# Performance work log

Measured on AMD Instinct MI355X. Metric: run time of the kernel, lower is better.

The kernel has to match this reference:

```python
import jax, jax.numpy as jnp
import numpy as np

HEAD_NUM = 4
EMB = 128
N_NODES = 50000
N_EDGES = 600000


def setup_inputs() -> dict:
    key = jax.random.key(0)
    k1, k2, k3, k4, k5, k6 = jax.random.split(key, 6)
    embeds = jax.random.normal(k1, (N_NODES, EMB), dtype=jnp.float32)
    qW = jax.random.normal(k2, (EMB, EMB), dtype=jnp.float32) * (1.0 / np.sqrt(EMB))
    kW = jax.random.normal(k3, (EMB, EMB), dtype=jnp.float32) * (1.0 / np.sqrt(EMB))
    vW = jax.random.normal(k4, (EMB, EMB), dtype=jnp.float32) * (1.0 / np.sqrt(EMB))
    rows = jax.random.randint(k5, (N_EDGES,), 0, N_NODES, dtype=jnp.int32)
    cols = jax.random.randint(k6, (N_EDGES,), 0, N_NODES, dtype=jnp.int32)
    return {"embeds": embeds, "qW": qW, "kW": kW, "vW": vW,
            "rows": rows, "cols": cols, "n_nodes": N_NODES}


def reference(embeds, qW, kW, vW, rows, cols, n_nodes):
    H = HEAD_NUM
    D = embeds.shape[1]
    Dh = D // H
    rowEmb = embeds[rows]                                   # [E, D] gather
    colEmb = embeds[cols]                                   # [E, D] gather
    q = (rowEmb @ qW).reshape(-1, H, Dh)                    # [E, H, Dh]
    k = (colEmb @ kW).reshape(-1, H, Dh)
    v = (colEmb @ vW).reshape(-1, H, Dh)
    att = jnp.einsum('ehd,ehd->eh', q, k)                   # per-edge per-head logits
    att = jnp.clip(att, -10.0, 10.0)
    expAtt = jnp.exp(att)                                   # [E, H]
    attNorm = jax.ops.segment_sum(expAtt, rows, num_segments=n_nodes)  # [N, H]
    att = expAtt / (attNorm[rows] + 1e-8)                   # segment softmax
    res = (att[..., None] * v).reshape(-1, D)               # [E, D]
    out = jax.ops.segment_sum(res, rows, num_segments=n_nodes)  # [N, D]
    return out
```

## Files before the change

kernel.cpp:

```cpp
#include <hip/hip_runtime.h>
#include <math.h>

#define EMB 128
#define HEADS 4
#define ROWSTRIDE 152
#define OSTRIDE2 388
#define CAP 64
#define CLAMP_L2 14.4269504088896f

typedef __attribute__((ext_vector_type(8))) _Float16 f16x8;
typedef __attribute__((ext_vector_type(4))) _Float16 f16x4;
typedef __attribute__((ext_vector_type(2))) _Float16 f16x2;
typedef __attribute__((ext_vector_type(4))) float f32x4;

__global__ __launch_bounds__(256) void prep_w(
    const float* __restrict__ Wq, const float* __restrict__ Wk, const float* __restrict__ Wv,
    _Float16* __restrict__ Wfrag)
{
    int flat = blockIdx.x * 256 + threadIdx.x;
    int m    = flat >> 14;
    int rem  = flat & 16383;
    int ct   = rem >> 11;
    int s    = (rem >> 9) & 3;
    int lane = (rem >> 3) & 63;
    int j    = rem & 7;
    int k = s * 32 + (lane >> 4) * 8 + j;
    int n = ct * 16 + (lane & 15);
    const float* Ws[3] = { Wq, Wk, Wv };
    float val = Ws[m][k * 128 + n];
    if (m == 0) val *= 1.44269504088896f;
    Wfrag[flat] = (_Float16)val;
}

__global__ __launch_bounds__(256) void mega_kernel(
    const float* __restrict__ embeds,
    const _Float16* __restrict__ Wfrag,
    _Float16* __restrict__ Qh, _Float16* __restrict__ KV,
    const int* __restrict__ rows, const int* __restrict__ cols,
    int* __restrict__ deg, unsigned short* __restrict__ slots,
    int N, int E, int PB, int S)
{
    __shared__ __align__(16) _Float16 sBuf[64 * OSTRIDE2];

    const int bid = blockIdx.x;
    const bool isProj = ((bid % S) == 0) && ((bid / S) < PB);

    if (!isProj) {
        int fidx = bid - min((bid + S - 1) / S, PB);
        int e = fidx * 256 + threadIdx.x;
        if (e < E) {
            int r = rows[e];
            int pos = atomicAdd(&deg[r], 1);
            if (pos < CAP) slots[(size_t)r * CAP + pos] = (unsigned short)cols[e];
        }
        return;
    }

    const int n0 = (bid / S) * 64;
    const int t  = threadIdx.x;

    #pragma unroll
    for (int j = 0; j < 8; j++) {
        int flat = t + j * 256;
        int row  = flat >> 5;
        int c4   = flat & 31;
        int gn   = n0 + row;
        float4 v = (gn < N) ? reinterpret_cast<const float4*>(embeds)[(size_t)gn * 32 + c4]
                            : make_float4(0.f, 0.f, 0.f, 0.f);
        f16x4 u = { (_Float16)v.x, (_Float16)v.y, (_Float16)v.z, (_Float16)v.w };
        *reinterpret_cast<f16x4*>(&sBuf[row * ROWSTRIDE + c4 * 4]) = u;
    }
    __syncthreads();

    const int w    = t >> 6;
    const int lane = t & 63;
    const int nlo  = lane & 15;
    const int quad = lane >> 4;

    f16x8 a[4][4];
    #pragma unroll
    for (int strip = 0; strip < 4; strip++)
        #pragma unroll
        for (int s = 0; s < 4; s++)
            a[strip][s] = *reinterpret_cast<const f16x8*>(
                &sBuf[(16 * strip + nlo) * ROWSTRIDE + s * 32 + quad * 8]);
    __syncthreads();

    const int rbase = quad * 4;

    #pragma unroll
    for (int u = 0; u < 6; u++) {
        const int T  = w + u * 4;
        const int m  = T >> 3;
        const int ct = T & 7;

        f16x8 b[4];
        #pragma unroll
        for (int s = 0; s < 4; s++)
            b[s] = *reinterpret_cast<const f16x8*>(
                Wfrag + ((size_t)(T * 4 + s) * 64 + lane) * 8);

        const int col  = ct * 16 + nlo;
        const int lcol = (m == 0) ? col
                                  : 128 + 8 * (col >> 2) + (col & 3) + ((m == 2) ? 4 : 0);

        #pragma unroll
        for (int strip = 0; strip < 4; strip++) {
            f32x4 acc = { 0.f, 0.f, 0.f, 0.f };
            #pragma unroll
            for (int s = 0; s < 4; s++)
                acc = __builtin_amdgcn_mfma_f32_16x16x32_f16(a[strip][s], b[s], acc, 0, 0, 0);
            const int row = 16 * strip + rbase;
            #pragma unroll
            for (int r = 0; r < 4; r++)
                sBuf[(row + r) * OSTRIDE2 + lcol] = (_Float16)acc[r];
        }
    }
    __syncthreads();

    #pragma unroll
    for (int j = 0; j < 4; j++) {
        int flat = j * 2048 + t * 8;
        int row  = flat >> 7;
        int col  = flat & 127;
        int gn   = n0 + row;
        if (gn < N) {
            f16x8 v = *reinterpret_cast<const f16x8*>(&sBuf[row * OSTRIDE2 + col]);
            *reinterpret_cast<f16x8*>(&Qh[(size_t)gn * EMB + col]) = v;
        }
    }
    #pragma unroll
    for (int j = 0; j < 8; j++) {
        int flat = j * 2048 + t * 8;
        int row  = flat >> 8;
        int col  = flat & 255;
        int gn   = n0 + row;
        if (gn < N) {
            f16x8 v = *reinterpret_cast<const f16x8*>(&sBuf[row * OSTRIDE2 + 128 + col]);
            *reinterpret_cast<f16x8*>(&KV[(size_t)gn * 256 + col]) = v;
        }
    }
}

__global__ __launch_bounds__(256) void node_fused(
    const _Float16* __restrict__ Qh, const _Float16* __restrict__ KV,
    const int* __restrict__ deg, const unsigned short* __restrict__ slots,
    float* __restrict__ out, int N)
{
    int n = blockIdx.x * 8 + (threadIdx.x >> 5);
    if (n >= N) return;
    int lane = threadIdx.x & 31;

    f16x4 qh = *reinterpret_cast<const f16x4*>(Qh + (size_t)n * EMB + lane * 4);
    f16x2 q01 = { qh.x, qh.y };
    f16x2 q23 = { qh.z, qh.w };

    int cnt = deg[n];
    if (cnt > CAP) cnt = CAP;
    const unsigned short* sl = slots + (size_t)n * CAP;
    const char* KVb = (const char*)KV;
    const unsigned loff = (unsigned)lane * 16u;

    float4 acc = make_float4(0.f, 0.f, 0.f, 0.f);
    float norm = 0.f;
    int i = 0;

    for (; i + 4 <= cnt; i += 4) {
        uint2 s4 = *reinterpret_cast<const uint2*>(sl + i);
        unsigned o0 = ((s4.x & 0xffffu) << 9) + loff;
        unsigned o1 = ((s4.x >> 16)     << 9) + loff;
        unsigned o2 = ((s4.y & 0xffffu) << 9) + loff;
        unsigned o3 = ((s4.y >> 16)     << 9) + loff;
        f16x8 kv0 = *reinterpret_cast<const f16x8*>(KVb + o0);
        f16x8 kv1 = *reinterpret_cast<const f16x8*>(KVb + o1);
        f16x8 kv2 = *reinterpret_cast<const f16x8*>(KVb + o2);
        f16x8 kv3 = *reinterpret_cast<const f16x8*>(KVb + o3);

        f16x2 k0a = __builtin_shufflevector(kv0, kv0, 0, 1);
        f16x2 k0b = __builtin_shufflevector(kv0, kv0, 2, 3);
        f16x2 k1a = __builtin_shufflevector(kv1, kv1, 0, 1);
        f16x2 k1b = __builtin_shufflevector(kv1, kv1, 2, 3);
        f16x2 k2a = __builtin_shufflevector(kv2, kv2, 0, 1);
        f16x2 k2b = __builtin_shufflevector(kv2, kv2, 2, 3);
        f16x2 k3a = __builtin_shufflevector(kv3, kv3, 0, 1);
        f16x2 k3b = __builtin_shufflevector(kv3, kv3, 2, 3);

        float d0 = __builtin_amdgcn_fdot2(k0a, q01, __builtin_amdgcn_fdot2(k0b, q23, 0.f, false), false);
        float d1 = __builtin_amdgcn_fdot2(k1a, q01, __builtin_amdgcn_fdot2(k1b, q23, 0.f, false), false);
        float d2 = __builtin_amdgcn_fdot2(k2a, q01, __builtin_amdgcn_fdot2(k2b, q23, 0.f, false), false);
        float d3 = __builtin_amdgcn_fdot2(k3a, q01, __builtin_amdgcn_fdot2(k3b, q23, 0.f, false), false);

        d0 += __shfl_xor(d0, 1); d1 += __shfl_xor(d1, 1); d2 += __shfl_xor(d2, 1); d3 += __shfl_xor(d3, 1);
        d0 += __shfl_xor(d0, 2); d1 += __shfl_xor(d1, 2); d2 += __shfl_xor(d2, 2); d3 += __shfl_xor(d3, 2);
        d0 += __shfl_xor(d0, 4); d1 += __shfl_xor(d1, 4); d2 += __shfl_xor(d2, 4); d3 += __shfl_xor(d3, 4);

        float ea0 = exp2f(fminf(CLAMP_L2, fmaxf(-CLAMP_L2, d0)));
        float ea1 = exp2f(fminf(CLAMP_L2, fmaxf(-CLAMP_L2, d1)));
        float ea2 = exp2f(fminf(CLAMP_L2, fmaxf(-CLAMP_L2, d2)));
        float ea3 = exp2f(fminf(CLAMP_L2, fmaxf(-CLAMP_L2, d3)));

        acc.x = fmaf(ea0, (float)kv0[4], acc.x);
        acc.y = fmaf(ea0, (float)kv0[5], acc.y);
        acc.z = fmaf(ea0, (float)kv0[6], acc.z);
        acc.w = fmaf(ea0, (float)kv0[7], acc.w);
        acc.x = fmaf(ea1, (float)kv1[4], acc.x);
        acc.y = fmaf(ea1, (float)kv1[5], acc.y);
        acc.z = fmaf(ea1, (float)kv1[6], acc.z);
        acc.w = fmaf(ea1, (float)kv1[7], acc.w);
        acc.x = fmaf(ea2, (float)kv2[4], acc.x);
        acc.y = fmaf(ea2, (float)kv2[5], acc.y);
        acc.z = fmaf(ea2, (float)kv2[6], acc.z);
        acc.w = fmaf(ea2, (float)kv2[7], acc.w);
        acc.x = fmaf(ea3, (float)kv3[4], acc.x);
        acc.y = fmaf(ea3, (float)kv3[5], acc.y);
        acc.z = fmaf(ea3, (float)kv3[6], acc.z);
        acc.w = fmaf(ea3, (float)kv3[7], acc.w);
        norm += ea0 + ea1 + ea2 + ea3;
    }
    for (; i < cnt; i++) {
        unsigned o0 = ((unsigned)sl[i] << 9) + loff;
        f16x8 kv0 = *reinterpret_cast<const f16x8*>(KVb + o0);
        f16x2 k0a = __builtin_shufflevector(kv0, kv0, 0, 1);
        f16x2 k0b = __builtin_shufflevector(kv0, kv0, 2, 3);
        float d0 = __builtin_amdgcn_fdot2(k0a, q01, __builtin_amdgcn_fdot2(k0b, q23, 0.f, false), false);
        d0 += __shfl_xor(d0, 1);
        d0 += __shfl_xor(d0, 2);
        d0 += __shfl_xor(d0, 4);
        float ea0 = exp2f(fminf(CLAMP_L2, fmaxf(-CLAMP_L2, d0)));
        acc.x = fmaf(ea0, (float)kv0[4], acc.x);
        acc.y = fmaf(ea0, (float)kv0[5], acc.y);
        acc.z = fmaf(ea0, (float)kv0[6], acc.z);
        acc.w = fmaf(ea0, (float)kv0[7], acc.w);
        norm += ea0;
    }

    float inv = 1.f / (norm + 1e-8f);
    acc.x *= inv; acc.y *= inv; acc.z *= inv; acc.w *= inv;
    reinterpret_cast<float4*>(out + (size_t)n * EMB)[lane] = acc;
}

extern "C" void kernel_launch(void* const* d_in, const int* in_sizes, int n_in,
                              void* d_out, int out_size, void* d_ws, size_t ws_size,
                              hipStream_t stream) {
    const float* embeds = (const float*)d_in[0];
    const float* qW     = (const float*)d_in[1];
    const float* kW     = (const float*)d_in[2];
    const float* vW     = (const float*)d_in[3];
    const int*   rows   = (const int*)d_in[4];
    const int*   cols   = (const int*)d_in[5];

    const int N = in_sizes[0] / EMB;
    const int E = in_sizes[4];

    _Float16*       Qh    = (_Float16*)d_ws;
    _Float16*       KV    = Qh + (size_t)N * EMB;
    _Float16*       Wfrag = KV + (size_t)N * 256;
    int*            deg   = (int*)(Wfrag + 3 * 16384);
    unsigned short* slots = (unsigned short*)(deg + N);

    float* out = (float*)d_out;

    (void)hipMemsetAsync(deg, 0, (size_t)N * sizeof(int), stream);

    prep_w<<<192, 256, 0, stream>>>(qW, kW, vW, Wfrag);

    const int PB = (N + 63) / 64;
    const int FB = (E + 255) / 256;
    const int S  = (PB + FB) / PB > 1 ? (PB + FB) / PB : 1;
    mega_kernel<<<PB + FB, 256, 0, stream>>>(embeds, Wfrag, Qh, KV,
                                             rows, cols, deg, slots, N, E, PB, S);

    node_fused<<<(N + 7) / 8, 256, 0, stream>>>(Qh, KV, deg, slots, out, N);
}
```

Baseline: 166.2 us.

## Shrink projection LDS buffer via staged K/V output and fold deg memset into prep

```diff
diff --git a/kernel.cpp b/kernel.cpp
--- a/kernel.cpp
+++ b/kernel.cpp
@@ -3,8 +3,7 @@
 
 #define EMB 128
 #define HEADS 4
-#define ROWSTRIDE 152
-#define OSTRIDE2 388
+#define OS 140
 #define CAP 64
 #define CLAMP_L2 14.4269504088896f
 
@@ -15,24 +14,27 @@
 
 __global__ __launch_bounds__(256) void prep_w(
     const float* __restrict__ Wq, const float* __restrict__ Wk, const float* __restrict__ Wv,
-    _Float16* __restrict__ Wfrag)
+    _Float16* __restrict__ Wfrag, int* __restrict__ deg, int N)
 {
     int flat = blockIdx.x * 256 + threadIdx.x;
-    int m    = flat >> 14;
-    int rem  = flat & 16383;
-    int ct   = rem >> 11;
-    int s    = (rem >> 9) & 3;
-    int lane = (rem >> 3) & 63;
-    int j    = rem & 7;
-    int k = s * 32 + (lane >> 4) * 8 + j;
-    int n = ct * 16 + (lane & 15);
-    const float* Ws[3] = { Wq, Wk, Wv };
-    float val = Ws[m][k * 128 + n];
-    if (m == 0) val *= 1.44269504088896f;
-    Wfrag[flat] = (_Float16)val;
-}
-
-__global__ __launch_bounds__(256) void mega_kernel(
+    if (flat < 3 * 16384) {
+        int m    = flat >> 14;
+        int rem  = flat & 16383;
+        int ct   = rem >> 11;
+        int s    = (rem >> 9) & 3;
+        int lane = (rem >> 3) & 63;
+        int j    = rem & 7;
+        int k = s * 32 + (lane >> 4) * 8 + j;
+        int n = ct * 16 + (lane & 15);
+        const float* Ws[3] = { Wq, Wk, Wv };
+        float val = Ws[m][k * 128 + n];
+        if (m == 0) val *= 1.44269504088896f;
+        Wfrag[flat] = (_Float16)val;
+    }
+    if (flat < N) deg[flat] = 0;
+}
+
+__global__ __launch_bounds__(256, 6) void mega_kernel(
     const float* __restrict__ embeds,
     const _Float16* __restrict__ Wfrag,
     _Float16* __restrict__ Qh, _Float16* __restrict__ KV,
@@ -40,7 +42,7 @@
     int* __restrict__ deg, unsigned short* __restrict__ slots,
     int N, int E, int PB, int S)
 {
-    __shared__ __align__(16) _Float16 sBuf[64 * OSTRIDE2];
+    __shared__ __align__(16) _Float16 sBuf[64 * OS];
 
     const int bid = blockIdx.x;
     const bool isProj = ((bid % S) == 0) && ((bid / S) < PB);
@@ -68,7 +70,7 @@
         float4 v = (gn < N) ? reinterpret_cast<const float4*>(embeds)[(size_t)gn * 32 + c4]
                             : make_float4(0.f, 0.f, 0.f, 0.f);
         f16x4 u = { (_Float16)v.x, (_Float16)v.y, (_Float16)v.z, (_Float16)v.w };
-        *reinterpret_cast<f16x4*>(&sBuf[row * ROWSTRIDE + c4 * 4]) = u;
+        *reinterpret_cast<f16x4*>(&sBuf[row * OS + c4 * 4]) = u;
     }
     __syncthreads();
 
@@ -83,27 +85,20 @@
         #pragma unroll
         for (int s = 0; s < 4; s++)
             a[strip][s] = *reinterpret_cast<const f16x8*>(
-                &sBuf[(16 * strip + nlo) * ROWSTRIDE + s * 32 + quad * 8]);
+                &sBuf[(16 * strip + nlo) * OS + s * 32 + quad * 8]);
     __syncthreads();
 
     const int rbase = quad * 4;
 
     #pragma unroll
-    for (int u = 0; u < 6; u++) {
-        const int T  = w + u * 4;
-        const int m  = T >> 3;
-        const int ct = T & 7;
-
+    for (int u = 0; u < 2; u++) {
+        const int ct = w * 2 + u;
         f16x8 b[4];
         #pragma unroll
         for (int s = 0; s < 4; s++)
             b[s] = *reinterpret_cast<const f16x8*>(
-                Wfrag + ((size_t)(T * 4 + s) * 64 + lane) * 8);
-
-        const int col  = ct * 16 + nlo;
-        const int lcol = (m == 0) ? col
-                                  : 128 + 8 * (col >> 2) + (col & 3) + ((m == 2) ? 4 : 0);
-
+                Wfrag + ((size_t)(ct * 4 + s) * 64 + lane) * 8);
+        const int lcol = ct * 16 + nlo;
         #pragma unroll
         for (int strip = 0; strip < 4; strip++) {
             f32x4 acc = { 0.f, 0.f, 0.f, 0.f };
@@ -113,11 +108,10 @@
             const int row = 16 * strip + rbase;
             #pragma unroll
             for (int r = 0; r < 4; r++)
-                sBuf[(row + r) * OSTRIDE2 + lcol] = (_Float16)acc[r];
+                sBuf[(row + r) * OS + lcol] = (_Float16)acc[r];
         }
     }
     __syncthreads();
-
     #pragma unroll
     for (int j = 0; j < 4; j++) {
         int flat = j * 2048 + t * 8;
@@ -125,19 +119,50 @@
         int col  = flat & 127;
         int gn   = n0 + row;
         if (gn < N) {
-            f16x8 v = *reinterpret_cast<const f16x8*>(&sBuf[row * OSTRIDE2 + col]);
+            f16x8 v = *reinterpret_cast<const f16x8*>(&sBuf[row * OS + col]);
             *reinterpret_cast<f16x8*>(&Qh[(size_t)gn * EMB + col]) = v;
         }
     }
-    #pragma unroll
-    for (int j = 0; j < 8; j++) {
-        int flat = j * 2048 + t * 8;
-        int row  = flat >> 8;
-        int col  = flat & 255;
-        int gn   = n0 + row;
-        if (gn < N) {
-            f16x8 v = *reinterpret_cast<const f16x8*>(&sBuf[row * OSTRIDE2 + 128 + col]);
-            *reinterpret_cast<f16x8*>(&KV[(size_t)gn * 256 + col]) = v;
+
+    #pragma unroll
+    for (int h = 0; h < 2; h++) {
+        __syncthreads();
+        const int m    = 1 + (w & 1);
+        const int voff = (m == 2) ? 4 : 0;
+        #pragma unroll
+        for (int u = 0; u < 2; u++) {
+            const int ct = 4 * h + (w >> 1) + 2 * u;
+            const int T  = m * 8 + ct;
+            f16x8 b[4];
+            #pragma unroll
+            for (int s = 0; s < 4; s++)
+                b[s] = *reinterpret_cast<const f16x8*>(
+                    Wfrag + ((size_t)(T * 4 + s) * 64 + lane) * 8);
+            const int colh = (ct - 4 * h) * 16 + nlo;
+            const int lidx = 8 * (colh >> 2) + (colh & 3) + voff;
+            #pragma unroll
+            for (int strip = 0; strip < 4; strip++) {
+                f32x4 acc = { 0.f, 0.f, 0.f, 0.f };
+                #pragma unroll
+                for (int s = 0; s < 4; s++)
+                    acc = __builtin_amdgcn_mfma_f32_16x16x32_f16(a[strip][s], b[s], acc, 0, 0, 0);
+                const int row = 16 * strip + rbase;
+                #pragma unroll
+                for (int r = 0; r < 4; r++)
+                    sBuf[(row + r) * OS + lidx] = (_Float16)acc[r];
+            }
+        }
+        __syncthreads();
+        #pragma unroll
+        for (int j = 0; j < 4; j++) {
+            int flat = j * 2048 + t * 8;
+            int row  = flat >> 7;
+            int col  = flat & 127;
+            int gn   = n0 + row;
+            if (gn < N) {
+                f16x8 v = *reinterpret_cast<const f16x8*>(&sBuf[row * OS + col]);
+                *reinterpret_cast<f16x8*>(&KV[(size_t)gn * 256 + 128 * h + col]) = v;
+            }
         }
     }
 }
@@ -260,9 +285,8 @@
 
     float* out = (float*)d_out;
 
-    (void)hipMemsetAsync(deg, 0, (size_t)N * sizeof(int), stream);
-
-    prep_w<<<192, 256, 0, stream>>>(qW, kW, vW, Wfrag);
+    const int GB = ((N > 3 * 16384 ? N : 3 * 16384) + 255) / 256;
+    prep_w<<<GB, 256, 0, stream>>>(qW, kW, vW, Wfrag, deg, N);
 
     const int PB = (N + 63) / 64;
     const int FB = (E + 255) / 256;
```

Result: slower. 224.5 us (+35.1%).
